# Kernel optimization log

Measured on AMD Instinct MI355X. Metric: run time of the kernel, lower is better.

The kernel has to match this reference:

```python
import jax, jax.numpy as jnp
import numpy as np

EMBED_DIM = 1024
NUM_HEADS = 16
HEAD_DIM = EMBED_DIM // NUM_HEADS


def setup_inputs() -> dict:
    key = jax.random.key(0)
    k_x, k_wqkv, k_bqkv, k_wp, k_bp = jax.random.split(key, 5)
    B, S, D = 2, 2048, EMBED_DIM
    bound_qkv = 1.0 / np.sqrt(D)
    bound_p = 1.0 / np.sqrt(D)
    return {
        "x": jax.random.normal(k_x, (B, S, D), dtype=jnp.float32),
        # torch nn.Linear stores weight as (out, in); keep that layout
        "w_qkv": jax.random.uniform(k_wqkv, (3 * D, D), jnp.float32, -bound_qkv, bound_qkv),
        "b_qkv": jax.random.uniform(k_bqkv, (3 * D,), jnp.float32, -bound_qkv, bound_qkv),
        "w_proj": jax.random.uniform(k_wp, (D, D), jnp.float32, -bound_p, bound_p),
        "b_proj": jax.random.uniform(k_bp, (D,), jnp.float32, -bound_p, bound_p),
    }


def reference(x, w_qkv, b_qkv, w_proj, b_proj):
    B, S, D = x.shape
    H, hd = NUM_HEADS, HEAD_DIM
    qkv = x @ w_qkv.T + b_qkv                      # [B,S,3D]
    qkv = qkv.reshape(B, S, 3, H, hd)
    qkv = jnp.transpose(qkv, (2, 0, 3, 1, 4))       # [3,B,H,S,hd]
    q, k, v = qkv[0], qkv[1], qkv[2]
    scale = 1.0 / np.sqrt(hd)
    scores = jnp.einsum('bhqd,bhkd->bhqk', q, k) * scale  # [B,H,S,S]
    attn = jax.nn.softmax(scores, axis=-1)
    out = jnp.einsum('bhqk,bhkd->bhqd', attn, v)    # [B,H,S,hd]
    out = jnp.transpose(out, (0, 2, 1, 3)).reshape(B, S, D)
    return out @ w_proj.T + b_proj
```

## Files before the change

kernel.cpp:

```cpp
#include <hip/hip_runtime.h>
#include <hip/hip_bf16.h>
#include <math.h>


typedef __bf16 bf16_t;
typedef __bf16 bf16x8 __attribute__((ext_vector_type(8)));
typedef __bf16 bf16x4v __attribute__((ext_vector_type(4)));
typedef float f32x4 __attribute__((ext_vector_type(4)));
typedef float f32x16 __attribute__((ext_vector_type(16)));

#define B_ 2
#define S_ 2048
#define D_ 1024
#define H_ 16
#define HD_ 64
#define QSCALE 0.18033688011112042f

__device__ __forceinline__ void load_lds16(const void* g, void* s) {
  __builtin_amdgcn_global_load_lds((__attribute__((address_space(1))) unsigned int*)g,
                                   (__attribute__((address_space(3))) unsigned int*)s,
                                   16, 0, 0);
}

__device__ __forceinline__ bf16_t fbf16(float x) {
  unsigned u = (__builtin_bit_cast(unsigned, x) + 0x8000u) >> 16;
  unsigned short s = (unsigned short)u;
  return __builtin_bit_cast(bf16_t, s);
}
__device__ __forceinline__ unsigned pack_bf16x2(float a, float b) {
  unsigned ua = __builtin_bit_cast(unsigned, a) + 0x8000u;
  unsigned ub = __builtin_bit_cast(unsigned, b) + 0x8000u;
  return __builtin_amdgcn_perm(ub, ua, 0x07060302u);
}

__global__ void tobf16_all(const float* __restrict__ x, const float* __restrict__ wq,
                           const float* __restrict__ wp, bf16_t* __restrict__ xb,
                           bf16_t* __restrict__ wqb, bf16_t* __restrict__ wpb) {
  int bid = blockIdx.x;
  const float* in;
  bf16_t* out;
  int base;
  if (bid < 4096) { in = x; out = xb; base = bid; }
  else if (bid < 7168) { in = wq; out = wqb; base = bid - 4096; }
  else { in = wp; out = wpb; base = bid - 7168; }
  int i = base * 256 + threadIdx.x;
  float4 v = ((const float4*)in)[i];
  uint2 o;
  o.x = pack_bf16x2(v.x, v.y);
  o.y = pack_bf16x2(v.z, v.w);
  ((uint2*)out)[i] = o;
}

template <int EPI, int BN>
__global__ __launch_bounds__(256, 2) void gemm_bt(
    const bf16_t* __restrict__ A, const bf16_t* __restrict__ Bm,
    const float* __restrict__ bias,
    bf16_t* __restrict__ qb, bf16_t* __restrict__ kb, bf16_t* __restrict__ vtb,
    float* __restrict__ outf) {
  constexpr int NI = BN / 32;
  constexpr int BUF = 8192 + BN * 64;
  __shared__ __align__(16) char smem[2 * BUF];
  const int tid = threadIdx.x;
  const int w = tid >> 6, lane = tid & 63;
  const int wm = w >> 1, wn = w & 1;
  const int quad = lane >> 4, l15 = lane & 15;
  const int m0 = blockIdx.y * 128, n0 = blockIdx.x * BN;

  auto stage = [&](int kt, int bb) {
    char* bA = smem + bb * BUF;
    char* bB = bA + 8192;
#pragma unroll
    for (int i = 0; i < 2; i++) {
      int ub = w * 128 + i * 64;
      int u = ub + lane;
      int r = u >> 2, c = (u & 3) ^ ((r >> 1) & 3);
      load_lds16(A + (size_t)(m0 + r) * 1024 + kt + c * 8, bA + (size_t)ub * 16);
    }
#pragma unroll
    for (int i = 0; i < BN / 64; i++) {
      int ub = w * (BN / 64) * 64 + i * 64;
      int u = ub + lane;
      int r = u >> 2, c = (u & 3) ^ ((r >> 1) & 3);
      load_lds16(Bm + (size_t)(n0 + r) * 1024 + kt + c * 8, bB + (size_t)ub * 16);
    }
  };

  f32x4 acc[4][NI];
#pragma unroll
  for (int mi = 0; mi < 4; mi++)
#pragma unroll
    for (int ni = 0; ni < NI; ni++) acc[mi][ni] = (f32x4){0.f, 0.f, 0.f, 0.f};

  stage(0, 0);

  for (int it = 0; it < 32; it++) {
    __syncthreads();
    if (it < 31) stage((it + 1) * 32, (it + 1) & 1);
    const bf16_t* bA = (const bf16_t*)(smem + (it & 1) * BUF);
    const bf16_t* bB = (const bf16_t*)(smem + (it & 1) * BUF + 8192);

    bf16x8 af[4], bfr[NI];
#pragma unroll
    for (int mi = 0; mi < 4; mi++) {
      int r = wm * 64 + mi * 16 + l15;
      af[mi] = *(const bf16x8*)(bA + (r * 4 + (quad ^ ((r >> 1) & 3))) * 8);
    }
#pragma unroll
    for (int ni = 0; ni < NI; ni++) {
      int r = wn * (BN / 2) + ni * 16 + l15;
      bfr[ni] = *(const bf16x8*)(bB + (r * 4 + (quad ^ ((r >> 1) & 3))) * 8);
    }
#pragma unroll
    for (int mi = 0; mi < 4; mi++)
#pragma unroll
      for (int ni = 0; ni < NI; ni++)
        acc[mi][ni] = __builtin_amdgcn_mfma_f32_16x16x32_bf16(af[mi], bfr[ni], acc[mi][ni], 0, 0, 0);
  }

#pragma unroll
  for (int mi = 0; mi < 4; mi++) {
#pragma unroll
    for (int ni = 0; ni < NI; ni++) {
      int n = n0 + wn * (BN / 2) + ni * 16 + l15;
      float bv = bias[n];
#pragma unroll
      for (int r = 0; r < 4; r++) {
        int m = m0 + wm * 64 + mi * 16 + quad * 4 + r;
        float v = acc[mi][ni][r] + bv;
        if (EPI == 0) {
          int t = n >> 10;
          int rr = n & 1023;
          int hh = rr >> 6, d = rr & 63;
          int bb = m >> 11, s = m & 2047;
          size_t bh = (size_t)(bb * H_ + hh);
          if (t == 0)
            qb[(bh * S_ + s) * HD_ + d] = fbf16(v * QSCALE);
          else if (t == 1)
            kb[(bh * S_ + s) * HD_ + d] = fbf16(v);
          else
            vtb[(bh * HD_ + d) * S_ + s] = fbf16(v);
        } else {
          outf[(size_t)m * 1024 + n] = v;
        }
      }
    }
  }
}

__global__ __launch_bounds__(128, 2) void attn(
    const bf16_t* __restrict__ qb, const bf16_t* __restrict__ kb,
    const bf16_t* __restrict__ vtb, bf16_t* __restrict__ ob) {
  __shared__ __align__(16) char smem[32768];
  const int tid = threadIdx.x, w = tid >> 6, lane = tid & 63;
  const int h2 = lane >> 5, l31 = lane & 31;
  const int xaddr = ((lane ^ 32) << 2);
  const int gid = blockIdx.x;
  const int g = gid & 7, k_ = gid >> 3;
  const int bh = g * 4 + (k_ >> 5);
  const int qt = k_ & 31;
  const int b = bh >> 4, h = bh & 15;
  const size_t base = (size_t)bh * S_ * HD_;
  const size_t vbase = (size_t)bh * HD_ * S_;
  const int q0 = qt * 64;
  const int myq = q0 + w * 32 + l31;

  bf16x8 bq[4];
#pragma unroll
  for (int ks = 0; ks < 4; ks++)
    bq[ks] = *(const bf16x8*)(qb + base + (size_t)myq * 64 + ks * 16 + h2 * 8);

  auto stage = [&](int kv0, int bb) {
    char* bK = smem + bb * 16384;
    char* bV = bK + 8192;
#pragma unroll
    for (int i = 0; i < 4; i++) {
      int ub = w * 256 + i * 64;
      int u = ub + lane;
      int r = u >> 3, c = (u & 7) ^ (r & 7);
      load_lds16(kb + base + (size_t)(kv0 + r) * 64 + c * 8, bK + (size_t)ub * 16);
      load_lds16(vtb + vbase + (size_t)r * S_ + kv0 + c * 8, bV + (size_t)ub * 16);
    }
  };

  f32x16 acc_o[2];
#pragma unroll
  for (int dt = 0; dt < 2; dt++)
#pragma unroll
    for (int i = 0; i < 16; i++) acc_o[dt][i] = 0.f;
  float l_acc = 0.f;

  stage(0, 0);

  for (int j = 0; j < 32; j++) {
    __syncthreads();
    if (j < 31) stage((j + 1) * 64, (j + 1) & 1);
    const bf16_t* bK = (const bf16_t*)(smem + (j & 1) * 16384);
    const bf16_t* bV = bK + 4096;

    f32x16 s_acc[2];
#pragma unroll
    for (int mt = 0; mt < 2; mt++)
#pragma unroll
      for (int i = 0; i < 16; i++) s_acc[mt][i] = 0.f;
#pragma unroll
    for (int ks = 0; ks < 4; ks++) {
#pragma unroll
      for (int mt = 0; mt < 2; mt++) {
        int r = mt * 32 + l31, c = ks * 2 + h2;
        bf16x8 ak = *(const bf16x8*)(bK + (r * 8 + (c ^ (r & 7))) * 8);
        s_acc[mt] = __builtin_amdgcn_mfma_f32_32x32x16_bf16(ak, bq[ks], s_acc[mt], 0, 0, 0);
      }
    }

    bf16x8 av[2][4];
#pragma unroll
    for (int ks = 0; ks < 4; ks++)
#pragma unroll
      for (int dt = 0; dt < 2; dt++) {
        int r = dt * 32 + l31, c = ks * 2 + h2;
        av[dt][ks] = *(const bf16x8*)(bV + (r * 8 + (c ^ (r & 7))) * 8);
      }

    unsigned pk[2][8];
    float ls = 0.f;
#pragma unroll
    for (int mt = 0; mt < 2; mt++)
#pragma unroll
      for (int i = 0; i < 8; i++) {
        float p0 = __builtin_amdgcn_exp2f(s_acc[mt][2 * i]);
        float p1 = __builtin_amdgcn_exp2f(s_acc[mt][2 * i + 1]);
        ls += p0 + p1;
        pk[mt][i] = pack_bf16x2(p0, p1);
      }
    l_acc += ls;

    bf16x8 bp[4];
#pragma unroll
    for (int mt = 0; mt < 2; mt++)
#pragma unroll
      for (int kk = 0; kk < 2; kk++) {
        unsigned a0 = pk[mt][kk * 4 + 0], a1 = pk[mt][kk * 4 + 1];
        unsigned a2 = pk[mt][kk * 4 + 2], a3 = pk[mt][kk * 4 + 3];
        unsigned r0 = (unsigned)__builtin_amdgcn_ds_bpermute(xaddr, (int)(h2 ? a0 : a2));
        unsigned r1 = (unsigned)__builtin_amdgcn_ds_bpermute(xaddr, (int)(h2 ? a1 : a3));
        union { unsigned u[4]; bf16x8 v; } bb;
        bb.u[0] = h2 ? r0 : a0;
        bb.u[1] = h2 ? r1 : a1;
        bb.u[2] = h2 ? a2 : r0;
        bb.u[3] = h2 ? a3 : r1;
        bp[mt * 2 + kk] = bb.v;
      }

#pragma unroll
    for (int ks = 0; ks < 4; ks++)
#pragma unroll
      for (int dt = 0; dt < 2; dt++)
        acc_o[dt] = __builtin_amdgcn_mfma_f32_32x32x16_bf16(av[dt][ks], bp[ks], acc_o[dt], 0, 0, 0);
  }

  float l_tot = l_acc + (float)__shfl_xor(l_acc, 32);
  float inv = 1.0f / l_tot;

#pragma unroll
  for (int dt = 0; dt < 2; dt++)
#pragma unroll
    for (int g4 = 0; g4 < 4; g4++) {
      uint2 o;
      o.x = pack_bf16x2(acc_o[dt][g4 * 4 + 0] * inv, acc_o[dt][g4 * 4 + 1] * inv);
      o.y = pack_bf16x2(acc_o[dt][g4 * 4 + 2] * inv, acc_o[dt][g4 * 4 + 3] * inv);
      int d = dt * 32 + g4 * 8 + h2 * 4;
      *(uint2*)(ob + ((size_t)b * S_ + myq) * D_ + h * HD_ + d) = o;
    }
}

extern "C" void kernel_launch(void* const* d_in, const int* in_sizes, int n_in,
                              void* d_out, int out_size, void* d_ws, size_t ws_size,
                              hipStream_t stream) {
  const float* x = (const float*)d_in[0];
  const float* w_qkv = (const float*)d_in[1];
  const float* b_qkv = (const float*)d_in[2];
  const float* w_proj = (const float*)d_in[3];
  const float* b_proj = (const float*)d_in[4];
  float* out = (float*)d_out;

  char* ws = (char*)d_ws;
  size_t off = 0;
  bf16_t* xb = (bf16_t*)(ws + off); off += (size_t)4096 * 1024 * 2;
  bf16_t* wqkvb = (bf16_t*)(ws + off); off += (size_t)3072 * 1024 * 2;
  bf16_t* wpb = (bf16_t*)(ws + off); off += (size_t)1024 * 1024 * 2;
  bf16_t* qb = (bf16_t*)(ws + off); off += (size_t)4096 * 1024 * 2;
  bf16_t* kb = (bf16_t*)(ws + off); off += (size_t)4096 * 1024 * 2;
  bf16_t* vtb = (bf16_t*)(ws + off); off += (size_t)4096 * 1024 * 2;
  bf16_t* ob = xb;

  tobf16_all<<<8192, 256, 0, stream>>>(x, w_qkv, w_proj, xb, wqkvb, wpb);
  gemm_bt<0, 128><<<dim3(24, 32), 256, 0, stream>>>(xb, wqkvb, b_qkv, qb, kb, vtb, nullptr);
  attn<<<1024, 128, 0, stream>>>(qb, kb, vtb, ob);
  gemm_bt<1, 64><<<dim3(16, 32), 256, 0, stream>>>(ob, wpb, b_proj, nullptr, nullptr, nullptr, out);
}
```

Baseline: 198.4 us.

## Software-pipeline QK^T of next tile with softmax and PV of current tile

```diff
diff --git a/kernel.cpp b/kernel.cpp
--- a/kernel.cpp
+++ b/kernel.cpp
@@ -190,28 +190,27 @@
   float l_acc = 0.f;
 
   stage(0, 0);
-
-  for (int j = 0; j < 32; j++) {
-    __syncthreads();
-    if (j < 31) stage((j + 1) * 64, (j + 1) & 1);
-    const bf16_t* bK = (const bf16_t*)(smem + (j & 1) * 16384);
-    const bf16_t* bV = bK + 4096;
-
-    f32x16 s_acc[2];
+  __syncthreads();
+  stage(64, 1);
+  f32x16 s_cur[2];
+  {
+    const bf16_t* bK = (const bf16_t*)smem;
 #pragma unroll
     for (int mt = 0; mt < 2; mt++)
 #pragma unroll
-      for (int i = 0; i < 16; i++) s_acc[mt][i] = 0.f;
-#pragma unroll
-    for (int ks = 0; ks < 4; ks++) {
+      for (int i = 0; i < 16; i++) s_cur[mt][i] = 0.f;
+#pragma unroll
+    for (int ks = 0; ks < 4; ks++)
 #pragma unroll
       for (int mt = 0; mt < 2; mt++) {
         int r = mt * 32 + l31, c = ks * 2 + h2;
         bf16x8 ak = *(const bf16x8*)(bK + (r * 8 + (c ^ (r & 7))) * 8);
-        s_acc[mt] = __builtin_amdgcn_mfma_f32_32x32x16_bf16(ak, bq[ks], s_acc[mt], 0, 0, 0);
-      }
-    }
-
+        s_cur[mt] = __builtin_amdgcn_mfma_f32_32x32x16_bf16(ak, bq[ks], s_cur[mt], 0, 0, 0);
+      }
+  }
+
+  for (int j = 0; j < 32; j++) {
+    const bf16_t* bV = (const bf16_t*)(smem + (j & 1) * 16384) + 4096;
     bf16x8 av[2][4];
 #pragma unroll
     for (int ks = 0; ks < 4; ks++)
@@ -221,14 +220,34 @@
         av[dt][ks] = *(const bf16x8*)(bV + (r * 8 + (c ^ (r & 7))) * 8);
       }
 
+    __syncthreads();
+    if (j < 30) stage((j + 2) * 64, j & 1);
+
+    f32x16 s_next[2];
+    if (j < 31) {
+      const bf16_t* bK1 = (const bf16_t*)(smem + ((j + 1) & 1) * 16384);
+#pragma unroll
+      for (int mt = 0; mt < 2; mt++)
+#pragma unroll
+        for (int i = 0; i < 16; i++) s_next[mt][i] = 0.f;
+#pragma unroll
+      for (int ks = 0; ks < 4; ks++)
+#pragma unroll
+        for (int mt = 0; mt < 2; mt++) {
+          int r = mt * 32 + l31, c = ks * 2 + h2;
+          bf16x8 ak = *(const bf16x8*)(bK1 + (r * 8 + (c ^ (r & 7))) * 8);
+          s_next[mt] = __builtin_amdgcn_mfma_f32_32x32x16_bf16(ak, bq[ks], s_next[mt], 0, 0, 0);
+        }
+    }
+
     unsigned pk[2][8];
     float ls = 0.f;
 #pragma unroll
     for (int mt = 0; mt < 2; mt++)
 #pragma unroll
       for (int i = 0; i < 8; i++) {
-        float p0 = __builtin_amdgcn_exp2f(s_acc[mt][2 * i]);
-        float p1 = __builtin_amdgcn_exp2f(s_acc[mt][2 * i + 1]);
+        float p0 = __builtin_amdgcn_exp2f(s_cur[mt][2 * i]);
+        float p1 = __builtin_amdgcn_exp2f(s_cur[mt][2 * i + 1]);
         ls += p0 + p1;
         pk[mt][i] = pack_bf16x2(p0, p1);
       }
@@ -256,6 +275,11 @@
 #pragma unroll
       for (int dt = 0; dt < 2; dt++)
         acc_o[dt] = __builtin_amdgcn_mfma_f32_32x32x16_bf16(av[dt][ks], bp[ks], acc_o[dt], 0, 0, 0);
+
+    if (j < 31) {
+      s_cur[0] = s_next[0];
+      s_cur[1] = s_next[1];
+    }
   }
 
   float l_tot = l_acc + (float)__shfl_xor(l_acc, 32);
```

Measured after the change: 194.4 us. -2.0%, faster.
